# Optimization experiments

Measured on AMD Instinct MI355X. Metric: run time of the kernel, lower is better.

## Reference

```python
import jax, jax.numpy as jnp
import numpy as np

B, T, F, H = 16, 1024, 1024, 16
D = F // H  # 64

def setup_inputs() -> dict:
    key = jax.random.key(0)
    k0, k1, k2 = jax.random.split(key, 3)
    return {
        "x": jax.random.normal(k0, (B, T, F), jnp.float32),
        "mask": jnp.zeros((B, 1, T, 1), jnp.float32),
        "W_attn": jax.random.normal(k1, (F, 3 * F), jnp.float32) * 0.02,
        "b_attn": jnp.zeros((3 * F,), jnp.float32),
        "W_proj": jax.random.normal(k2, (F, F), jnp.float32) * 0.02,
        "b_proj": jnp.zeros((F,), jnp.float32),
    }

def reference(x, mask, W_attn, b_attn, W_proj, b_proj):
    # qkv projection (Conv1D == linear with transposed weight layout)
    qkv = x @ W_attn + b_attn                       # [B,T,3F]
    q, k, v = jnp.split(qkv, 3, axis=-1)
    split = lambda t: t.reshape(B, T, H, D).transpose(0, 2, 1, 3)  # [B,H,T,D]
    q, k, v = split(q), split(k), split(v)
    # non-standard: contract over T -> [B,H,D,D] score matrix
    s = jnp.einsum('bhtd,bhte->bhde', q, k) / jnp.sqrt(jnp.float32(D))
    tril = jnp.tril(jnp.ones((D, D), bool))         # bias buffer sliced to DxD
    s = jnp.where(tril, s, jnp.float32(-10000.0))
    # second matmul with V (before softmax), scaled by dk^2
    w = jnp.einsum('bhde,bhte->bhtd', s, v) / (jnp.float32(D) ** 2)  # [B,H,T,D]
    w = jax.nn.softmax(w + mask, axis=-2)           # softmax over T (dim=-2)
    a = w * v                                        # elementwise, not weighted sum
    merge = lambda t: t.transpose(0, 2, 1, 3).reshape(B, T, F)
    a = merge(a) @ W_proj + b_proj                   # output projection
    return a, merge(w)
```

## Files before the change

### kernel.cpp

```cpp
#include <hip/hip_runtime.h>
#include <math.h>

namespace {
constexpr int B = 16, T = 1024, F = 1024, H = 16, D = 64;
constexpr int NT = B * T;
constexpr int QKV_COLS = 3 * F;

constexpr size_t XHI_OFF = 0;
constexpr size_t XLO_OFF = 33554432;
constexpr size_t WAH_OFF = 67108864;
constexpr size_t WVL_OFF = 73400320;
constexpr size_t QB_OFF  = 75497472;
constexpr size_t KB_OFF  = 109051904;
constexpr size_t SB_OFF  = 142606336;
constexpr size_t AB_OFF  = 146800640;
constexpr size_t WPB_OFF = 180355072;
constexpr size_t VB_OFF   = QB_OFF;
constexpr size_t WRAW_OFF = XHI_OFF;
constexpr size_t SP_OFF   = WVL_OFF;
}

typedef __attribute__((ext_vector_type(8))) __bf16 bf16x8;
typedef __attribute__((ext_vector_type(4))) float f32x4;

__device__ __forceinline__ unsigned short f2bf(float f) {
  unsigned u = __builtin_bit_cast(unsigned, f);
  u += 0x7FFFu + ((u >> 16) & 1u);
  return (unsigned short)(u >> 16);
}
__device__ __forceinline__ float bf2f(unsigned short s) {
  return __builtin_bit_cast(float, (unsigned)s << 16);
}
__device__ __forceinline__ void gld16(const unsigned short* g, unsigned short* l) {
  __builtin_amdgcn_global_load_lds(
      (const __attribute__((address_space(1))) unsigned int*)g,
      (__attribute__((address_space(3))) unsigned int*)l, 16, 0, 0);
}

__global__ __launch_bounds__(256) void cast_x(const float* __restrict__ x,
                                              unsigned short* __restrict__ xhi,
                                              unsigned short* __restrict__ xlo) {
  int i = (blockIdx.x * 256 + threadIdx.x) * 4;
  float4 v = *(const float4*)&x[i];
  ushort4 h, l;
  h.x = f2bf(v.x); l.x = f2bf(v.x - bf2f(h.x));
  h.y = f2bf(v.y); l.y = f2bf(v.y - bf2f(h.y));
  h.z = f2bf(v.z); l.z = f2bf(v.z - bf2f(h.z));
  h.w = f2bf(v.w); l.w = f2bf(v.w - bf2f(h.w));
  *(ushort4*)&xhi[i] = h;
  *(ushort4*)&xlo[i] = l;
}

__global__ __launch_bounds__(256) void tcast(const float* __restrict__ W,
                                             unsigned short* __restrict__ Wt,
                                             unsigned short* __restrict__ Wlo,
                                             int ncols, int locol0) {
  __shared__ float tile[64][65];
  const int bx = blockIdx.x, by = blockIdx.y, tid = threadIdx.x;
#pragma unroll
  for (int i = 0; i < 16; ++i) {
    int idx = tid + i * 256;
    int r = idx >> 6, c = idx & 63;
    tile[r][c] = W[(size_t)(by * 64 + r) * ncols + bx * 64 + c];
  }
  __syncthreads();
#pragma unroll
  for (int i = 0; i < 16; ++i) {
    int idx = tid + i * 256;
    int r = idx >> 6, c = idx & 63;
    int col = bx * 64 + r;
    float w = tile[c][r];
    unsigned short h = f2bf(w);
    Wt[(size_t)col * 1024 + by * 64 + c] = h;
    if (col >= locol0) {
      Wlo[(size_t)(col - locol0) * 1024 + by * 64 + c] = f2bf(w - bf2f(h));
    }
  }
}

__global__ __launch_bounds__(256) void qk_mfma(
    const unsigned short* __restrict__ A, const unsigned short* __restrict__ Bt,
    const float* __restrict__ ba, unsigned short* __restrict__ qb,
    unsigned short* __restrict__ kb) {
  __shared__ __align__(16) unsigned short Alds[4096];
  __shared__ __align__(16) unsigned short Blds[4096];
  const int tid = threadIdx.x;
  const int wave = tid >> 6, lane = tid & 63;
  const int quad = lane >> 4, m16 = lane & 15;
  const int wr = wave >> 1, wc = wave & 1;
  const int row0 = blockIdx.y * 128, col0 = blockIdx.x * 128;
  const int mA = tid & 127, hi = tid >> 7;
  const unsigned short* Abase = A + (size_t)(row0 + mA) * 1024 + hi * 8;
  const unsigned short* Bbase = Bt + (size_t)(col0 + mA) * 1024 + hi * 8;
  f32x4 acc[4][4] = {};
  for (int kc = 0; kc < 1024; kc += 32) {
    gld16(Abase + kc,      &Alds[wave * 512]);
    gld16(Abase + kc + 16, &Alds[2048 + wave * 512]);
    gld16(Bbase + kc,      &Blds[wave * 512]);
    gld16(Bbase + kc + 16, &Blds[2048 + wave * 512]);
    __syncthreads();
    bf16x8 af[4], bfr[4];
#pragma unroll
    for (int mi = 0; mi < 4; ++mi)
      af[mi] = *(const bf16x8*)&Alds[quad * 1024 + (wr * 64 + mi * 16 + m16) * 8];
#pragma unroll
    for (int ni = 0; ni < 4; ++ni)
      bfr[ni] = *(const bf16x8*)&Blds[quad * 1024 + (wc * 64 + ni * 16 + m16) * 8];
#pragma unroll
    for (int mi = 0; mi < 4; ++mi)
#pragma unroll
      for (int ni = 0; ni < 4; ++ni)
        acc[mi][ni] = __builtin_amdgcn_mfma_f32_16x16x32_bf16(
            af[mi], bfr[ni], acc[mi][ni], 0, 0, 0);
    __syncthreads();
  }
  const int part = col0 >> 10;
#pragma unroll
  for (int mi = 0; mi < 4; ++mi) {
#pragma unroll
    for (int ni = 0; ni < 4; ++ni) {
      int gcol = col0 + wc * 64 + ni * 16 + m16;
      int f = gcol & 1023;
      int h = f >> 6, dd = f & 63;
      float bias = ba[gcol];
#pragma unroll
      for (int r = 0; r < 4; ++r) {
        int grow = row0 + wr * 64 + mi * 16 + quad * 4 + r;
        int b = grow >> 10, t = grow & 1023;
        size_t hidx = (((size_t)b * H + h) * T + t) * D + dd;
        float val = acc[mi][ni][r] + bias;
        if (part == 0) qb[hidx] = f2bf(val);
        else kb[hidx] = f2bf(val);
      }
    }
  }
}

__global__ __launch_bounds__(256) void v_mfma(
    const unsigned short* __restrict__ Ah, const unsigned short* __restrict__ Al,
    const unsigned short* __restrict__ Bh, const unsigned short* __restrict__ Bl,
    const float* __restrict__ ba, float* __restrict__ vb) {
  __shared__ __align__(16) unsigned short AldsH[4096];
  __shared__ __align__(16) unsigned short AldsL[4096];
  __shared__ __align__(16) unsigned short BldsH[4096];
  __shared__ __align__(16) unsigned short BldsL[4096];
  const int tid = threadIdx.x;
  const int wave = tid >> 6, lane = tid & 63;
  const int quad = lane >> 4, m16 = lane & 15;
  const int wr = wave >> 1, wc = wave & 1;
  const int row0 = blockIdx.y * 128, col0 = blockIdx.x * 128;
  const int mA = tid & 127, hi = tid >> 7;
  const size_t aoff = (size_t)(row0 + mA) * 1024 + hi * 8;
  const size_t boff = (size_t)(col0 + mA) * 1024 + hi * 8;
  f32x4 acc[4][4] = {};
  for (int kc = 0; kc < 1024; kc += 32) {
    gld16(Ah + aoff + kc,      &AldsH[wave * 512]);
    gld16(Ah + aoff + kc + 16, &AldsH[2048 + wave * 512]);
    gld16(Al + aoff + kc,      &AldsL[wave * 512]);
    gld16(Al + aoff + kc + 16, &AldsL[2048 + wave * 512]);
    gld16(Bh + boff + kc,      &BldsH[wave * 512]);
    gld16(Bh + boff + kc + 16, &BldsH[2048 + wave * 512]);
    gld16(Bl + boff + kc,      &BldsL[wave * 512]);
    gld16(Bl + boff + kc + 16, &BldsL[2048 + wave * 512]);
    __syncthreads();
#pragma unroll
    for (int mi = 0; mi < 4; ++mi) {
      int aidx = quad * 1024 + (wr * 64 + mi * 16 + m16) * 8;
      bf16x8 ah = *(const bf16x8*)&AldsH[aidx];
      bf16x8 al = *(const bf16x8*)&AldsL[aidx];
#pragma unroll
      for (int ni = 0; ni < 4; ++ni) {
        int bidx = quad * 1024 + (wc * 64 + ni * 16 + m16) * 8;
        bf16x8 bh = *(const bf16x8*)&BldsH[bidx];
        bf16x8 bl = *(const bf16x8*)&BldsL[bidx];
        acc[mi][ni] = __builtin_amdgcn_mfma_f32_16x16x32_bf16(ah, bh, acc[mi][ni], 0, 0, 0);
        acc[mi][ni] = __builtin_amdgcn_mfma_f32_16x16x32_bf16(ah, bl, acc[mi][ni], 0, 0, 0);
        acc[mi][ni] = __builtin_amdgcn_mfma_f32_16x16x32_bf16(al, bh, acc[mi][ni], 0, 0, 0);
      }
    }
    __syncthreads();
  }
#pragma unroll
  for (int mi = 0; mi < 4; ++mi) {
#pragma unroll
    for (int ni = 0; ni < 4; ++ni) {
      int gcol = col0 + wc * 64 + ni * 16 + m16;
      int h = gcol >> 6, dd = gcol & 63;
      float bias = ba[2048 + gcol];
#pragma unroll
      for (int r = 0; r < 4; ++r) {
        int grow = row0 + wr * 64 + mi * 16 + quad * 4 + r;
        int b = grow >> 10, t = grow & 1023;
        vb[(((size_t)b * H + h) * T + t) * D + dd] = acc[mi][ni][r] + bias;
      }
    }
  }
}

__global__ __launch_bounds__(256) void proj_mfma(
    const unsigned short* __restrict__ A, const unsigned short* __restrict__ Bt,
    const float* __restrict__ bp, float* __restrict__ out1) {
  __shared__ __align__(16) unsigned short Alds[4096];
  __shared__ __align__(16) unsigned short Blds[4096];
  const int tid = threadIdx.x;
  const int wave = tid >> 6, lane = tid & 63;
  const int quad = lane >> 4, m16 = lane & 15;
  const int wr = wave >> 1, wc = wave & 1;
  const int row0 = blockIdx.y * 128, col0 = blockIdx.x * 128;
  const int mA = tid & 127, hi = tid >> 7;
  const unsigned short* Abase = A + (size_t)(row0 + mA) * 1024 + hi * 8;
  const unsigned short* Bbase = Bt + (size_t)(col0 + mA) * 1024 + hi * 8;
  f32x4 acc[4][4] = {};
  for (int kc = 0; kc < 1024; kc += 32) {
    gld16(Abase + kc,      &Alds[wave * 512]);
    gld16(Abase + kc + 16, &Alds[2048 + wave * 512]);
    gld16(Bbase + kc,      &Blds[wave * 512]);
    gld16(Bbase + kc + 16, &Blds[2048 + wave * 512]);
    __syncthreads();
    bf16x8 af[4], bfr[4];
#pragma unroll
    for (int mi = 0; mi < 4; ++mi)
      af[mi] = *(const bf16x8*)&Alds[quad * 1024 + (wr * 64 + mi * 16 + m16) * 8];
#pragma unroll
    for (int ni = 0; ni < 4; ++ni)
      bfr[ni] = *(const bf16x8*)&Blds[quad * 1024 + (wc * 64 + ni * 16 + m16) * 8];
#pragma unroll
    for (int mi = 0; mi < 4; ++mi)
#pragma unroll
      for (int ni = 0; ni < 4; ++ni)
        acc[mi][ni] = __builtin_amdgcn_mfma_f32_16x16x32_bf16(
            af[mi], bfr[ni], acc[mi][ni], 0, 0, 0);
    __syncthreads();
  }
#pragma unroll
  for (int mi = 0; mi < 4; ++mi) {
#pragma unroll
    for (int ni = 0; ni < 4; ++ni) {
      int gcol = col0 + wc * 64 + ni * 16 + m16;
      float bias = bp[gcol];
#pragma unroll
      for (int r = 0; r < 4; ++r) {
        int grow = row0 + wr * 64 + mi * 16 + quad * 4 + r;
        out1[(size_t)grow * F + gcol] = acc[mi][ni][r] + bias;
      }
    }
  }
}

__global__ __launch_bounds__(256) void score_kernel(
    const unsigned short* __restrict__ qb, const unsigned short* __restrict__ kb,
    float* __restrict__ sb) {
  __shared__ float qs[64][65];
  __shared__ float ks[64][65];
  const int bh = blockIdx.x;
  const int tid = threadIdx.x;
  const size_t base = (size_t)bh * T * D;
  const int d0 = (tid >> 4) * 4, e0 = (tid & 15) * 4;
  float acc[4][4] = {};
  for (int ch = 0; ch < T / 64; ++ch) {
#pragma unroll
    for (int i = 0; i < 4; ++i) {
      int idx = (tid + i * 256) * 4;
      ushort4 qv = *(const ushort4*)&qb[base + (size_t)ch * 4096 + idx];
      ushort4 kv = *(const ushort4*)&kb[base + (size_t)ch * 4096 + idx];
      int r = idx >> 6, c = idx & 63;
      qs[r][c] = bf2f(qv.x); qs[r][c+1] = bf2f(qv.y);
      qs[r][c+2] = bf2f(qv.z); qs[r][c+3] = bf2f(qv.w);
      ks[r][c] = bf2f(kv.x); ks[r][c+1] = bf2f(kv.y);
      ks[r][c+2] = bf2f(kv.z); ks[r][c+3] = bf2f(kv.w);
    }
    __syncthreads();
#pragma unroll 8
    for (int tt = 0; tt < 64; ++tt) {
      float qa[4], kv[4];
#pragma unroll
      for (int i = 0; i < 4; ++i) qa[i] = qs[tt][d0 + i];
#pragma unroll
      for (int j = 0; j < 4; ++j) kv[j] = ks[tt][e0 + j];
#pragma unroll
      for (int i = 0; i < 4; ++i)
#pragma unroll
        for (int j = 0; j < 4; ++j) acc[i][j] += qa[i] * kv[j];
    }
    __syncthreads();
  }
#pragma unroll
  for (int i = 0; i < 4; ++i) {
#pragma unroll
    for (int j = 0; j < 4; ++j) {
      int dd = d0 + i, ee = e0 + j;
      float v = acc[i][j] * 0.125f;
      if (ee > dd) v = -10000.0f;
      sb[(size_t)bh * (D * D) + dd * D + ee] = v;
    }
  }
}

__global__ __launch_bounds__(256) void exp_kernel(
    const float* __restrict__ vb, const float* __restrict__ sb,
    const float* __restrict__ mask, float* __restrict__ wraw,
    float* __restrict__ sp) {
  const int tc = blockIdx.x, bh = blockIdx.y;
  const int b = bh >> 4;
  const int tid = threadIdx.x;
  const int lane = tid & 63;
  const int dg = __builtin_amdgcn_readfirstlane(tid >> 6);
  const int tg = tc * 64 + lane;
  const float* vrow = vb + (size_t)bh * (T * D) + (size_t)tg * D;
  float4 vreg[16];
#pragma unroll
  for (int i = 0; i < 16; ++i) vreg[i] = *(const float4*)&vrow[i * 4];
  const float mval = mask[(size_t)b * T + tg];
  float ex[16];
#pragma unroll
  for (int dd = 0; dd < 16; ++dd) {
    const int d = dg * 16 + dd;
    const float* srow = sb + (size_t)bh * 4096 + (size_t)d * 64;
    float acc = 0.f;
#pragma unroll
    for (int e4 = 0; e4 < 16; ++e4) {
      float4 s4 = *(const float4*)&srow[e4 * 4];
      acc += s4.x * vreg[e4].x + s4.y * vreg[e4].y +
             s4.z * vreg[e4].z + s4.w * vreg[e4].w;
    }
    float w = acc * (1.0f / 4096.0f) + mval;
    ex[dd] = __expf(w);
    wraw[(size_t)bh * (T * D) + (size_t)d * T + tg] = ex[dd];
  }
#pragma unroll
  for (int dd = 0; dd < 16; ++dd) {
    float v = ex[dd];
    v += __shfl_xor(v, 1, 64);
    v += __shfl_xor(v, 2, 64);
    v += __shfl_xor(v, 4, 64);
    v += __shfl_xor(v, 8, 64);
    v += __shfl_xor(v, 16, 64);
    v += __shfl_xor(v, 32, 64);
    if (lane == 0) sp[((size_t)bh * 16 + tc) * 64 + dg * 16 + dd] = v;
  }
}

__global__ __launch_bounds__(256) void norm_kernel(
    const float* __restrict__ vb, const float* __restrict__ wraw,
    const float* __restrict__ sp, unsigned short* __restrict__ ab,
    float* __restrict__ out2) {
  __shared__ float wt[64][65];
  __shared__ float invS[64];
  const int tc = blockIdx.x, bh = blockIdx.y;
  const int b = bh >> 4, h = bh & 15;
  const int tid = threadIdx.x;
  if (tid < 64) {
    float S = 0.f;
#pragma unroll
    for (int j = 0; j < 16; ++j) S += sp[((size_t)bh * 16 + j) * 64 + tid];
    invS[tid] = 1.0f / S;
  }
#pragma unroll
  for (int i = 0; i < 16; ++i) {
    int idx = tid + i * 256;
    int dd = idx >> 6, tt = idx & 63;
    wt[dd][tt] = wraw[(size_t)bh * (T * D) + (size_t)dd * T + tc * 64 + tt];
  }
  __syncthreads();
  const int d = tid & 63, trow = tid >> 6;
#pragma unroll
  for (int j = 0; j < 16; ++j) {
    int tl = trow * 16 + j;
    int tg = tc * 64 + tl;
    float o = wt[d][tl] * invS[d];
    float vv = vb[(size_t)bh * (T * D) + (size_t)tg * D + d];
    size_t oidx = ((size_t)b * T + tg) * F + h * 64 + d;
    out2[oidx] = o;
    ab[oidx] = f2bf(o * vv);
  }
}

extern "C" void kernel_launch(void* const* d_in, const int* in_sizes, int n_in,
                              void* d_out, int out_size, void* d_ws,
                              size_t ws_size, hipStream_t stream) {
  const float* x = (const float*)d_in[0];
  const float* mask = (const float*)d_in[1];
  const float* Wa = (const float*)d_in[2];
  const float* ba = (const float*)d_in[3];
  const float* Wp = (const float*)d_in[4];
  const float* bp = (const float*)d_in[5];
  char* ws = (char*)d_ws;
  float* out = (float*)d_out;

  unsigned short* xhi = (unsigned short*)(ws + XHI_OFF);
  unsigned short* xlo = (unsigned short*)(ws + XLO_OFF);
  unsigned short* Wah = (unsigned short*)(ws + WAH_OFF);
  unsigned short* Wvl = (unsigned short*)(ws + WVL_OFF);
  unsigned short* qb  = (unsigned short*)(ws + QB_OFF);
  unsigned short* kb  = (unsigned short*)(ws + KB_OFF);
  float* sb   = (float*)(ws + SB_OFF);
  unsigned short* ab  = (unsigned short*)(ws + AB_OFF);
  unsigned short* Wpb = (unsigned short*)(ws + WPB_OFF);
  float* vb   = (float*)(ws + VB_OFF);
  float* wraw = (float*)(ws + WRAW_OFF);
  float* sp   = (float*)(ws + SP_OFF);

  cast_x<<<NT * F / 1024, 256, 0, stream>>>(x, xhi, xlo);
  tcast<<<dim3(QKV_COLS / 64, F / 64), 256, 0, stream>>>(Wa, Wah, Wvl,
                                                         QKV_COLS, 2048);
  tcast<<<dim3(F / 64, F / 64), 256, 0, stream>>>(Wp, Wpb, Wvl, F, 1 << 30);

  qk_mfma<<<dim3(2048 / 128, NT / 128), 256, 0, stream>>>(xhi, Wah, ba, qb, kb);

  score_kernel<<<dim3(B * H), 256, 0, stream>>>(qb, kb, sb);

  v_mfma<<<dim3(F / 128, NT / 128), 256, 0, stream>>>(
      xhi, xlo, Wah + (size_t)2048 * 1024, Wvl, ba, vb);

  exp_kernel<<<dim3(T / 64, B * H), 256, 0, stream>>>(vb, sb, mask, wraw, sp);

  norm_kernel<<<dim3(T / 64, B * H), 256, 0, stream>>>(
      vb, wraw, sp, ab, out + (size_t)NT * F);

  proj_mfma<<<dim3(F / 128, NT / 128), 256, 0, stream>>>(ab, Wpb, bp, out);
}
```

Before: 759.9 us.

## Unify GEMMs into double-buffered 256x256 MFMA kernel with swizzled LDS

Replaces the three separate 128x128 GEMM kernels (QK, split-precision V, output projection) with one templated 256x256-tile, 512-thread kernel. It double-buffers LDS with async global-to-LDS loads and explicit vmcnt waits, and XOR-swizzles the LDS layout to avoid bank conflicts. The V GEMM's three hi/lo products become 96 sequential K-tiles over concatenated operand segments. Larger tiles raise data reuse and overlap loads with MFMA work, at the cost of more registers and LDS per block, fewer blocks, and fragile hand-written waitcnt and barrier sequencing.

```diff
diff --git a/kernel.cpp b/kernel.cpp
--- a/kernel.cpp
+++ b/kernel.cpp
@@ -78,170 +78,145 @@
   }
 }
 
-__global__ __launch_bounds__(256) void qk_mfma(
-    const unsigned short* __restrict__ A, const unsigned short* __restrict__ Bt,
-    const float* __restrict__ ba, unsigned short* __restrict__ qb,
-    unsigned short* __restrict__ kb) {
-  __shared__ __align__(16) unsigned short Alds[4096];
-  __shared__ __align__(16) unsigned short Blds[4096];
+__device__ __forceinline__ void stage256(const unsigned short* __restrict__ Ag,
+                                         const unsigned short* __restrict__ Bg,
+                                         int row0, int col0, int kin,
+                                         unsigned short* lbase, int wave,
+                                         int lane) {
+  const int rsub = lane >> 3;
+  const int logb = ((lane & 7) ^ rsub) << 4;
+  const int isB = logb >> 6;
+  const int koff = kin + ((logb & 63) >> 1);
+#pragma unroll
+  for (int L = 0; L < 4; ++L) {
+    const int R0 = (L * 8 + wave) * 8;
+    const int r = R0 + rsub;
+    const unsigned short* src =
+        isB ? (Bg + (size_t)(col0 + r) * 1024 + koff)
+            : (Ag + (size_t)(row0 + r) * 1024 + koff);
+    gld16(src, lbase + (size_t)R0 * 64);
+  }
+}
+
+template <int MODE>
+__global__ __launch_bounds__(512, 2) void gemm256(
+    const unsigned short* __restrict__ A0, const unsigned short* __restrict__ A1,
+    const unsigned short* __restrict__ B0, const unsigned short* __restrict__ B1,
+    const float* __restrict__ bias, void* __restrict__ out0,
+    void* __restrict__ out1) {
+  __shared__ __align__(16) unsigned short lds[2][256][64];
   const int tid = threadIdx.x;
   const int wave = tid >> 6, lane = tid & 63;
-  const int quad = lane >> 4, m16 = lane & 15;
-  const int wr = wave >> 1, wc = wave & 1;
-  const int row0 = blockIdx.y * 128, col0 = blockIdx.x * 128;
-  const int mA = tid & 127, hi = tid >> 7;
-  const unsigned short* Abase = A + (size_t)(row0 + mA) * 1024 + hi * 8;
-  const unsigned short* Bbase = Bt + (size_t)(col0 + mA) * 1024 + hi * 8;
-  f32x4 acc[4][4] = {};
-  for (int kc = 0; kc < 1024; kc += 32) {
-    gld16(Abase + kc,      &Alds[wave * 512]);
-    gld16(Abase + kc + 16, &Alds[2048 + wave * 512]);
-    gld16(Bbase + kc,      &Blds[wave * 512]);
-    gld16(Bbase + kc + 16, &Blds[2048 + wave * 512]);
-    __syncthreads();
-    bf16x8 af[4], bfr[4];
-#pragma unroll
-    for (int mi = 0; mi < 4; ++mi)
-      af[mi] = *(const bf16x8*)&Alds[quad * 1024 + (wr * 64 + mi * 16 + m16) * 8];
-#pragma unroll
-    for (int ni = 0; ni < 4; ++ni)
-      bfr[ni] = *(const bf16x8*)&Blds[quad * 1024 + (wc * 64 + ni * 16 + m16) * 8];
-#pragma unroll
-    for (int mi = 0; mi < 4; ++mi)
-#pragma unroll
-      for (int ni = 0; ni < 4; ++ni)
-        acc[mi][ni] = __builtin_amdgcn_mfma_f32_16x16x32_bf16(
-            af[mi], bfr[ni], acc[mi][ni], 0, 0, 0);
-    __syncthreads();
-  }
-  const int part = col0 >> 10;
-#pragma unroll
-  for (int mi = 0; mi < 4; ++mi) {
-#pragma unroll
-    for (int ni = 0; ni < 4; ++ni) {
-      int gcol = col0 + wc * 64 + ni * 16 + m16;
-      int f = gcol & 1023;
-      int h = f >> 6, dd = f & 63;
-      float bias = ba[gcol];
-#pragma unroll
-      for (int r = 0; r < 4; ++r) {
-        int grow = row0 + wr * 64 + mi * 16 + quad * 4 + r;
-        int b = grow >> 10, t = grow & 1023;
-        size_t hidx = (((size_t)b * H + h) * T + t) * D + dd;
-        float val = acc[mi][ni][r] + bias;
-        if (part == 0) qb[hidx] = f2bf(val);
-        else kb[hidx] = f2bf(val);
-      }
-    }
-  }
-}
-
-__global__ __launch_bounds__(256) void v_mfma(
-    const unsigned short* __restrict__ Ah, const unsigned short* __restrict__ Al,
-    const unsigned short* __restrict__ Bh, const unsigned short* __restrict__ Bl,
-    const float* __restrict__ ba, float* __restrict__ vb) {
-  __shared__ __align__(16) unsigned short AldsH[4096];
-  __shared__ __align__(16) unsigned short AldsL[4096];
-  __shared__ __align__(16) unsigned short BldsH[4096];
-  __shared__ __align__(16) unsigned short BldsL[4096];
-  const int tid = threadIdx.x;
-  const int wave = tid >> 6, lane = tid & 63;
-  const int quad = lane >> 4, m16 = lane & 15;
-  const int wr = wave >> 1, wc = wave & 1;
-  const int row0 = blockIdx.y * 128, col0 = blockIdx.x * 128;
-  const int mA = tid & 127, hi = tid >> 7;
-  const size_t aoff = (size_t)(row0 + mA) * 1024 + hi * 8;
-  const size_t boff = (size_t)(col0 + mA) * 1024 + hi * 8;
-  f32x4 acc[4][4] = {};
-  for (int kc = 0; kc < 1024; kc += 32) {
-    gld16(Ah + aoff + kc,      &AldsH[wave * 512]);
-    gld16(Ah + aoff + kc + 16, &AldsH[2048 + wave * 512]);
-    gld16(Al + aoff + kc,      &AldsL[wave * 512]);
-    gld16(Al + aoff + kc + 16, &AldsL[2048 + wave * 512]);
-    gld16(Bh + boff + kc,      &BldsH[wave * 512]);
-    gld16(Bh + boff + kc + 16, &BldsH[2048 + wave * 512]);
-    gld16(Bl + boff + kc,      &BldsL[wave * 512]);
-    gld16(Bl + boff + kc + 16, &BldsL[2048 + wave * 512]);
-    __syncthreads();
-#pragma unroll
-    for (int mi = 0; mi < 4; ++mi) {
-      int aidx = quad * 1024 + (wr * 64 + mi * 16 + m16) * 8;
-      bf16x8 ah = *(const bf16x8*)&AldsH[aidx];
-      bf16x8 al = *(const bf16x8*)&AldsL[aidx];
-#pragma unroll
-      for (int ni = 0; ni < 4; ++ni) {
-        int bidx = quad * 1024 + (wc * 64 + ni * 16 + m16) * 8;
-        bf16x8 bh = *(const bf16x8*)&BldsH[bidx];
-        bf16x8 bl = *(const bf16x8*)&BldsL[bidx];
-        acc[mi][ni] = __builtin_amdgcn_mfma_f32_16x16x32_bf16(ah, bh, acc[mi][ni], 0, 0, 0);
-        acc[mi][ni] = __builtin_amdgcn_mfma_f32_16x16x32_bf16(ah, bl, acc[mi][ni], 0, 0, 0);
-        acc[mi][ni] = __builtin_amdgcn_mfma_f32_16x16x32_bf16(al, bh, acc[mi][ni], 0, 0, 0);
-      }
-    }
-    __syncthreads();
-  }
-#pragma unroll
-  for (int mi = 0; mi < 4; ++mi) {
-#pragma unroll
-    for (int ni = 0; ni < 4; ++ni) {
-      int gcol = col0 + wc * 64 + ni * 16 + m16;
-      int h = gcol >> 6, dd = gcol & 63;
-      float bias = ba[2048 + gcol];
-#pragma unroll
-      for (int r = 0; r < 4; ++r) {
-        int grow = row0 + wr * 64 + mi * 16 + quad * 4 + r;
-        int b = grow >> 10, t = grow & 1023;
-        vb[(((size_t)b * H + h) * T + t) * D + dd] = acc[mi][ni][r] + bias;
-      }
-    }
-  }
-}
-
-__global__ __launch_bounds__(256) void proj_mfma(
-    const unsigned short* __restrict__ A, const unsigned short* __restrict__ Bt,
-    const float* __restrict__ bp, float* __restrict__ out1) {
-  __shared__ __align__(16) unsigned short Alds[4096];
-  __shared__ __align__(16) unsigned short Blds[4096];
-  const int tid = threadIdx.x;
-  const int wave = tid >> 6, lane = tid & 63;
-  const int quad = lane >> 4, m16 = lane & 15;
-  const int wr = wave >> 1, wc = wave & 1;
-  const int row0 = blockIdx.y * 128, col0 = blockIdx.x * 128;
-  const int mA = tid & 127, hi = tid >> 7;
-  const unsigned short* Abase = A + (size_t)(row0 + mA) * 1024 + hi * 8;
-  const unsigned short* Bbase = Bt + (size_t)(col0 + mA) * 1024 + hi * 8;
-  f32x4 acc[4][4] = {};
-  for (int kc = 0; kc < 1024; kc += 32) {
-    gld16(Abase + kc,      &Alds[wave * 512]);
-    gld16(Abase + kc + 16, &Alds[2048 + wave * 512]);
-    gld16(Bbase + kc,      &Blds[wave * 512]);
-    gld16(Bbase + kc + 16, &Blds[2048 + wave * 512]);
-    __syncthreads();
-    bf16x8 af[4], bfr[4];
-#pragma unroll
-    for (int mi = 0; mi < 4; ++mi)
-      af[mi] = *(const bf16x8*)&Alds[quad * 1024 + (wr * 64 + mi * 16 + m16) * 8];
-#pragma unroll
-    for (int ni = 0; ni < 4; ++ni)
-      bfr[ni] = *(const bf16x8*)&Blds[quad * 1024 + (wc * 64 + ni * 16 + m16) * 8];
-#pragma unroll
-    for (int mi = 0; mi < 4; ++mi)
-#pragma unroll
-      for (int ni = 0; ni < 4; ++ni)
-        acc[mi][ni] = __builtin_amdgcn_mfma_f32_16x16x32_bf16(
-            af[mi], bfr[ni], acc[mi][ni], 0, 0, 0);
-    __syncthreads();
-  }
-#pragma unroll
-  for (int mi = 0; mi < 4; ++mi) {
-#pragma unroll
-    for (int ni = 0; ni < 4; ++ni) {
-      int gcol = col0 + wc * 64 + ni * 16 + m16;
-      float bias = bp[gcol];
-#pragma unroll
-      for (int r = 0; r < 4; ++r) {
-        int grow = row0 + wr * 64 + mi * 16 + quad * 4 + r;
-        out1[(size_t)grow * F + gcol] = acc[mi][ni][r] + bias;
+  const int wr = wave >> 2, wc = wave & 3;
+  const int m16 = lane & 15, quad = lane >> 4;
+  const int row0 = blockIdx.y * 256, col0 = blockIdx.x * 256;
+  constexpr int NKT = (MODE == 1) ? 96 : 32;
+  f32x4 acc[8][4] = {};
+
+  stage256(A0, B0, row0, col0, 0, &lds[0][0][0], wave, lane);
+
+  int cur = 0;
+  for (int kt = 0; kt < NKT; ++kt) {
+    if (kt + 1 < NKT) {
+      const unsigned short* Ag = A0;
+      const unsigned short* Bg = B0;
+      int kin;
+      if constexpr (MODE == 1) {
+        const int kn = kt + 1, seg = kn >> 5;
+        kin = (kn & 31) << 5;
+        if (seg == 1) Ag = A1;
+        if (seg == 2) Bg = B1;
+      } else {
+        kin = (kt + 1) << 5;
+      }
+      stage256(Ag, Bg, row0, col0, kin, &lds[cur ^ 1][0][0], wave, lane);
+      asm volatile("s_waitcnt vmcnt(4)" ::: "memory");
+    } else {
+      asm volatile("s_waitcnt vmcnt(0)" ::: "memory");
+    }
+    __builtin_amdgcn_s_barrier();
+
+    const char* tb = (const char*)&lds[cur][0][0];
+#pragma unroll
+    for (int ph = 0; ph < 2; ++ph) {
+      bf16x8 af[4], bfr[4];
+#pragma unroll
+      for (int i = 0; i < 4; ++i) {
+        const int r = wr * 128 + (ph * 4 + i) * 16 + m16;
+        af[i] = *(const bf16x8*)(tb + r * 128 +
+                                 ((quad * 16) ^ ((r & 7) << 4)));
+      }
+#pragma unroll
+      for (int j = 0; j < 4; ++j) {
+        const int c = wc * 64 + j * 16 + m16;
+        bfr[j] = *(const bf16x8*)(tb + c * 128 +
+                                  ((64 + quad * 16) ^ ((c & 7) << 4)));
+      }
+      __builtin_amdgcn_s_barrier();
+      asm volatile("s_waitcnt lgkmcnt(0)" ::: "memory");
+      __builtin_amdgcn_sched_barrier(0);
+      __builtin_amdgcn_s_setprio(1);
+#pragma unroll
+      for (int i = 0; i < 4; ++i)
+#pragma unroll
+        for (int j = 0; j < 4; ++j)
+          acc[ph * 4 + i][j] = __builtin_amdgcn_mfma_f32_16x16x32_bf16(
+              af[i], bfr[j], acc[ph * 4 + i][j], 0, 0, 0);
+      __builtin_amdgcn_s_setprio(0);
+      __builtin_amdgcn_s_barrier();
+    }
+    cur ^= 1;
+  }
+
+  if constexpr (MODE == 0) {
+    unsigned short* dst = (col0 >= 1024) ? (unsigned short*)out1
+                                         : (unsigned short*)out0;
+#pragma unroll
+    for (int j = 0; j < 4; ++j) {
+      const int gcol = col0 + wc * 64 + j * 16 + m16;
+      const int f = gcol & 1023;
+      const int h = f >> 6, dd = f & 63;
+      const float bv = bias[gcol];
+#pragma unroll
+      for (int i = 0; i < 8; ++i) {
+#pragma unroll
+        for (int r = 0; r < 4; ++r) {
+          const int grow = row0 + wr * 128 + i * 16 + quad * 4 + r;
+          const int b = grow >> 10, t = grow & 1023;
+          dst[(((size_t)b * H + h) * T + t) * D + dd] = f2bf(acc[i][j][r] + bv);
+        }
+      }
+    }
+  } else if constexpr (MODE == 1) {
+    float* vbp = (float*)out0;
+#pragma unroll
+    for (int j = 0; j < 4; ++j) {
+      const int f = col0 + wc * 64 + j * 16 + m16;
+      const int h = f >> 6, dd = f & 63;
+      const float bv = bias[f];
+#pragma unroll
+      for (int i = 0; i < 8; ++i) {
+#pragma unroll
+        for (int r = 0; r < 4; ++r) {
+          const int grow = row0 + wr * 128 + i * 16 + quad * 4 + r;
+          const int b = grow >> 10, t = grow & 1023;
+          vbp[(((size_t)b * H + h) * T + t) * D + dd] = acc[i][j][r] + bv;
+        }
+      }
+    }
+  } else {
+    float* o = (float*)out0;
+#pragma unroll
+    for (int j = 0; j < 4; ++j) {
+      const int gcol = col0 + wc * 64 + j * 16 + m16;
+      const float bv = bias[gcol];
+#pragma unroll
+      for (int i = 0; i < 8; ++i) {
+#pragma unroll
+        for (int r = 0; r < 4; ++r) {
+          const int grow = row0 + wr * 128 + i * 16 + quad * 4 + r;
+          o[(size_t)grow * F + gcol] = acc[i][j][r] + bv;
+        }
       }
     }
   }
@@ -405,17 +380,19 @@
                                                          QKV_COLS, 2048);
   tcast<<<dim3(F / 64, F / 64), 256, 0, stream>>>(Wp, Wpb, Wvl, F, 1 << 30);
 
-  qk_mfma<<<dim3(2048 / 128, NT / 128), 256, 0, stream>>>(xhi, Wah, ba, qb, kb);
+  gemm256<0><<<dim3(2048 / 256, NT / 256), 512, 0, stream>>>(
+      xhi, nullptr, Wah, nullptr, ba, qb, kb);
 
   score_kernel<<<dim3(B * H), 256, 0, stream>>>(qb, kb, sb);
 
-  v_mfma<<<dim3(F / 128, NT / 128), 256, 0, stream>>>(
-      xhi, xlo, Wah + (size_t)2048 * 1024, Wvl, ba, vb);
+  gemm256<1><<<dim3(F / 256, NT / 256), 512, 0, stream>>>(
+      xhi, xlo, Wah + (size_t)2048 * 1024, Wvl, ba + 2048, vb, nullptr);
 
   exp_kernel<<<dim3(T / 64, B * H), 256, 0, stream>>>(vb, sb, mask, wraw, sp);
 
   norm_kernel<<<dim3(T / 64, B * H), 256, 0, stream>>>(
       vb, wraw, sp, ab, out + (size_t)NT * F);
 
-  proj_mfma<<<dim3(F / 128, NT / 128), 256, 0, stream>>>(ab, Wpb, bp, out);
-}
+  gemm256<2><<<dim3(F / 256, NT / 256), 512, 0, stream>>>(
+      ab, nullptr, Wpb, nullptr, bp, out, nullptr);
+}
```

New measurement: 638.4 us. 16.0% less time.
